# Kernel optimization log

Hardware: AMD Instinct MI355X
Metric: run time of the kernel (lower is better)

Reference implementation:

```python
import jax, jax.numpy as jnp
import numpy as np

R, I, T = 1024, 8, 65536
SPECTRAL_RADIUS = 1.0
CONNECTIVITY_RATE = 1.0


def setup_inputs() -> dict:
    key = jax.random.key(0)
    k1, k2, k3, k4 = jax.random.split(key, 4)
    inputs = jax.random.normal(k1, (T, I), dtype=jnp.float32)
    W_in = jax.random.uniform(k2, (R, I), minval=-1.0, maxval=1.0, dtype=jnp.float32)
    # reservoir: uniform(-1,1), sparsified where a random normal exceeds connectivity_rate
    W = jax.random.uniform(k3, (R, R), minval=-1.0, maxval=1.0, dtype=jnp.float32)
    mask_noise = jax.random.normal(k4, (R, R), dtype=jnp.float32)
    W = jnp.where(mask_noise > CONNECTIVITY_RATE, 0.0, W)
    # scale to target spectral radius (init-time, done in numpy)
    rho = np.max(np.abs(np.linalg.eigvals(np.asarray(W, dtype=np.float64))))
    W_res = (W * (SPECTRAL_RADIUS / np.float32(rho))).astype(jnp.float32)
    state0 = jnp.zeros((R,), dtype=jnp.float32)
    return {"inputs": inputs, "W_in": W_in, "W_res": W_res, "state0": state0}


def reference(inputs, W_in, W_res, state0):
    # ESN reservoir scan: s_t = tanh(W_in @ x_t + W_res @ s_{t-1});
    # collect [s_t; x_t] as column t of the state collection matrix.
    def step(s, x):
        s_new = jnp.tanh(W_in @ x + W_res @ s)  # (R,)
        return s_new, jnp.concatenate([s_new, x])  # (R + I,)

    _, cols = jax.lax.scan(step, state0, inputs)  # cols: (T, R + I)
    return cols.T  # (R + I, T), matching column-wise tf.concat
```

## Files before the change

### kernel.cpp

```cpp
#include <hip/hip_runtime.h>
#include <cstdint>

typedef __attribute__((ext_vector_type(8))) short short8;
typedef __attribute__((ext_vector_type(4))) float f32x4;
typedef __attribute__((ext_vector_type(4))) unsigned u32x4;

#define R_DIM 1024
#define KE    1056
#define T_LEN 65536
#define LCH   64
#define WARM  24
#define STEPS (WARM + LCH)
#define CGN   32
#define WGC   32
#define RWG   8

static __device__ __forceinline__ unsigned short f2bf(float f){
  unsigned u = __builtin_bit_cast(unsigned, f);
  u += 0x7fffu + ((u >> 16) & 1u);
  return (unsigned short)(u >> 16);
}
static __device__ __forceinline__ float fast_tanh(float x){
  float e = __expf(2.0f * x);
  return 1.0f - 2.0f / (e + 1.0f);
}

__global__ void k_build_wext(const float* __restrict__ Wres,
                             const float* __restrict__ Win,
                             short* __restrict__ Wext){
  int idx = blockIdx.x * 256 + threadIdx.x;
  int r = idx / KE, k = idx % KE;
  float v = 0.0f;
  if (k < 1024)      v = Wres[(size_t)r * 1024 + k];
  else if (k < 1032) v = Win[r * 8 + (k - 1024)];
  Wext[idx] = (short)f2bf(v);
}

__global__ void k_zero(unsigned* __restrict__ p){
  p[blockIdx.x * 256 + threadIdx.x] = 0u;
}

__global__ void k_init_x(const float* __restrict__ in, short* __restrict__ S0,
                         unsigned* __restrict__ cnt){
  int c = blockIdx.x * 256 + threadIdx.x;
  if (c < 512) cnt[c] = 0u;
  if (c < 1024){
    int t0 = c * LCH - WARM;
    uint4 xv = {0,0,0,0};
    if (t0 >= 0){
      const float4 A4 = *(const float4*)(in + (size_t)t0 * 8);
      const float4 B4 = *(const float4*)(in + (size_t)t0 * 8 + 4);
      xv.x = f2bf(A4.x) | ((unsigned)f2bf(A4.y) << 16);
      xv.y = f2bf(A4.z) | ((unsigned)f2bf(A4.w) << 16);
      xv.z = f2bf(B4.x) | ((unsigned)f2bf(B4.y) << 16);
      xv.w = f2bf(B4.z) | ((unsigned)f2bf(B4.w) << 16);
    }
    *(uint4*)(S0 + (size_t)c * KE + 1024) = xv;
  }
}

__global__ void k_xrows(const float* __restrict__ in, float* __restrict__ out){
  int t = blockIdx.x * 256 + threadIdx.x;
  const float4 a = *(const float4*)(in + (size_t)t * 8);
  const float4 b = *(const float4*)(in + (size_t)t * 8 + 4);
  out[(size_t)(R_DIM + 0) * T_LEN + t] = a.x;
  out[(size_t)(R_DIM + 1) * T_LEN + t] = a.y;
  out[(size_t)(R_DIM + 2) * T_LEN + t] = a.z;
  out[(size_t)(R_DIM + 3) * T_LEN + t] = a.w;
  out[(size_t)(R_DIM + 4) * T_LEN + t] = b.x;
  out[(size_t)(R_DIM + 5) * T_LEN + t] = b.y;
  out[(size_t)(R_DIM + 6) * T_LEN + t] = b.z;
  out[(size_t)(R_DIM + 7) * T_LEN + t] = b.w;
}

__global__ void k_transpose(const short* __restrict__ hist, float* __restrict__ out){
  __shared__ float tile[64][65];
  const int t0 = blockIdx.x * 64;
  const int r0 = blockIdx.y * 64;
  for (int it = 0; it < 2; ++it){
    int id = it * 256 + threadIdx.x;
    int tr = id >> 3;
    int c8 = (id & 7) * 8;
    short8 v = *(const short8*)(hist + (size_t)(t0 + tr) * KE + r0 + c8);
    #pragma unroll
    for (int j = 0; j < 8; ++j){
      unsigned u = ((unsigned)(unsigned short)v[j]) << 16;
      tile[tr][c8 + j] = __builtin_bit_cast(float, u);
    }
  }
  __syncthreads();
  #pragma unroll
  for (int p = 0; p < 16; ++p){
    int rr = (threadIdx.x >> 6) + p * 4;
    int tc = threadIdx.x & 63;
    out[(size_t)(r0 + rr) * T_LEN + t0 + tc] = tile[tc][rr];
  }
}

template<bool HIST>
__global__ __launch_bounds__(512, 1)
void k_esn(const float* __restrict__ inputs, const short* __restrict__ Wext,
           short* __restrict__ S0, short* __restrict__ S1,
           short* __restrict__ hist, unsigned* __restrict__ cnt,
           float* __restrict__ out)
{
  __shared__ __align__(16) char lds[65536];
  const int tid  = threadIdx.x;
  const int cg   = blockIdx.x & (CGN - 1);
  const int rwg  = blockIdx.x >> 5;
  const int wv   = tid >> 6;
  const int lane = tid & 63;
  const int l15  = lane & 15, l4 = lane >> 4;
  const int hi   = wv & 1;
  const int rbase = rwg * 128 + (wv >> 1) * 32;
  const int colbase = cg * WGC;
  unsigned* gflags = cnt + cg * 16;

  auto browf = [&](int col, int k) -> const short* {
    if (!HIST || k <= WARM) return ((k & 1) ? S1 : S0) + (size_t)col * KE;
    return hist + (size_t)(col * LCH + (k - WARM) - 1) * KE;
  };
  auto wrowf = [&](int col, int k) -> short* {
    if (!HIST || (k + 1) <= WARM) return ((k & 1) ? S0 : S1) + (size_t)col * KE;
    return hist + (size_t)(col * LCH + (k - WARM)) * KE;
  };

  const int NA = hi ? 16 : 17;
  const int KB = hi ? 17 : 0;
  const int NL = hi ? 15 : 17;
  short8 a0[17], a1[17];
  {
    const short* abase = Wext + (size_t)(rbase + l15) * KE + l4 * 8;
    #pragma unroll
    for (int i = 0; i < 17; ++i){
      if (i < NA){
        const short* ap = abase + (KB + i) * 32;
        a0[i] = *(const short8*)ap;
        a1[i] = *(const short8*)(ap + (size_t)16 * KE);
      }
    }
  }

  const int scol = tid >> 4;
  const int skb0 = (tid & 15) << 4;
  const int sswz = (scol & 7) << 4;
  const int colb0 = l15 * 2048;
  const int bswz  = (l15 & 7) << 4;
  const int l4b   = l4 * 16;

  for (int k = 0; k < STEPS; ++k){
    if (k > 0){
      if (wv == 0){
        const unsigned* fp = gflags + (lane & 7);
        int guard = 0;
        for (;;){
          unsigned v;
          asm volatile("global_load_dword %0, %1, off sc0 sc1\n\t"
                       "s_waitcnt vmcnt(0)"
                       : "=v"(v) : "v"(fp) : "memory");
          if (!__any((int)(v < (unsigned)k))) break;
          __builtin_amdgcn_s_sleep(1);
          if (++guard > 1000000) break;
        }
      }
      __syncthreads();
    }

    unsigned long long t00=0, t01=0, t10=0, t11=0;
    if (hi){
      const unsigned long long* tp0 =
        (const unsigned long long*)(browf(colbase + l15, k) + 1024 + l4 * 8);
      const unsigned long long* tp1 =
        (const unsigned long long*)(browf(colbase + 16 + l15, k) + 1024 + l4 * 8);
      t00 = __hip_atomic_load(tp0,     __ATOMIC_RELAXED, __HIP_MEMORY_SCOPE_AGENT);
      t01 = __hip_atomic_load(tp0 + 1, __ATOMIC_RELAXED, __HIP_MEMORY_SCOPE_AGENT);
      t10 = __hip_atomic_load(tp1,     __ATOMIC_RELAXED, __HIP_MEMORY_SCOPE_AGENT);
      t11 = __hip_atomic_load(tp1 + 1, __ATOMIC_RELAXED, __HIP_MEMORY_SCOPE_AGENT);
    }

    {
      const short* srow = browf(colbase + scol, k);
      const char* sp = (const char*)srow + skb0;
      u32x4 r0,r1,r2,r3,r4,r5,r6,r7;
      asm volatile(
        "global_load_dwordx4 %0, %8, off sc0 sc1\n\t"
        "global_load_dwordx4 %1, %8, off offset:256 sc0 sc1\n\t"
        "global_load_dwordx4 %2, %8, off offset:512 sc0 sc1\n\t"
        "global_load_dwordx4 %3, %8, off offset:768 sc0 sc1\n\t"
        "global_load_dwordx4 %4, %8, off offset:1024 sc0 sc1\n\t"
        "global_load_dwordx4 %5, %8, off offset:1280 sc0 sc1\n\t"
        "global_load_dwordx4 %6, %8, off offset:1536 sc0 sc1\n\t"
        "global_load_dwordx4 %7, %8, off offset:1792 sc0 sc1\n\t"
        "s_waitcnt vmcnt(0)"
        : "=&v"(r0),"=&v"(r1),"=&v"(r2),"=&v"(r3),
          "=&v"(r4),"=&v"(r5),"=&v"(r6),"=&v"(r7)
        : "v"(sp) : "memory");
      char* dst = &lds[scol * 2048];
      *(u32x4*)(dst + ((skb0 +    0) ^ sswz)) = r0;
      *(u32x4*)(dst + ((skb0 +  256) ^ sswz)) = r1;
      *(u32x4*)(dst + ((skb0 +  512) ^ sswz)) = r2;
      *(u32x4*)(dst + ((skb0 +  768) ^ sswz)) = r3;
      *(u32x4*)(dst + ((skb0 + 1024) ^ sswz)) = r4;
      *(u32x4*)(dst + ((skb0 + 1280) ^ sswz)) = r5;
      *(u32x4*)(dst + ((skb0 + 1536) ^ sswz)) = r6;
      *(u32x4*)(dst + ((skb0 + 1792) ^ sswz)) = r7;
    }
    __syncthreads();

    f32x4 acc00 = {0,0,0,0}, acc01 = {0,0,0,0}, acc10 = {0,0,0,0}, acc11 = {0,0,0,0};
    #pragma unroll
    for (int i = 0; i < 17; ++i){
      if (i < NL){
        int kb = (KB + i) * 64 + l4b;
        const short8 b0 = *(const short8*)(&lds[colb0 + ((kb) ^ bswz)]);
        const short8 b1 = *(const short8*)(&lds[colb0 + 32768 + ((kb) ^ bswz)]);
        acc00 = __builtin_amdgcn_mfma_f32_16x16x32_bf16(a0[i], b0, acc00, 0, 0, 0);
        acc01 = __builtin_amdgcn_mfma_f32_16x16x32_bf16(a0[i], b1, acc01, 0, 0, 0);
        acc10 = __builtin_amdgcn_mfma_f32_16x16x32_bf16(a1[i], b0, acc10, 0, 0, 0);
        acc11 = __builtin_amdgcn_mfma_f32_16x16x32_bf16(a1[i], b1, acc11, 0, 0, 0);
      }
    }
    if (hi){
      u32x4 v0; v0.x=(unsigned)t00; v0.y=(unsigned)(t00>>32); v0.z=(unsigned)t01; v0.w=(unsigned)(t01>>32);
      u32x4 v1; v1.x=(unsigned)t10; v1.y=(unsigned)(t10>>32); v1.z=(unsigned)t11; v1.w=(unsigned)(t11>>32);
      const short8 b0 = __builtin_bit_cast(short8, v0);
      const short8 b1 = __builtin_bit_cast(short8, v1);
      acc00 = __builtin_amdgcn_mfma_f32_16x16x32_bf16(a0[15], b0, acc00, 0, 0, 0);
      acc01 = __builtin_amdgcn_mfma_f32_16x16x32_bf16(a0[15], b1, acc01, 0, 0, 0);
      acc10 = __builtin_amdgcn_mfma_f32_16x16x32_bf16(a1[15], b0, acc10, 0, 0, 0);
      acc11 = __builtin_amdgcn_mfma_f32_16x16x32_bf16(a1[15], b1, acc11, 0, 0, 0);
    }

    __syncthreads();
    {
      f32x4 wA = hi ? acc00 : acc10;
      f32x4 wB = hi ? acc01 : acc11;
      char* xp = &lds[wv * 2048 + lane * 32];
      *(f32x4*)(xp)      = wA;
      *(f32x4*)(xp + 16) = wB;
    }
    __syncthreads();
    {
      const char* pp = &lds[(wv ^ 1) * 2048 + lane * 32];
      f32x4 p0 = *(const f32x4*)(pp);
      f32x4 p1 = *(const f32x4*)(pp + 16);
      f32x4 f0 = (hi ? acc10 : acc00) + p0;
      f32x4 f1 = (hi ? acc11 : acc01) + p1;
      const int rowb = rbase + hi * 16 + l4 * 4;
      #pragma unroll
      for (int ct = 0; ct < 2; ++ct){
        f32x4 z = ct ? f1 : f0;
        float s0 = fast_tanh(z[0]), s1 = fast_tanh(z[1]);
        float s2 = fast_tanh(z[2]), s3 = fast_tanh(z[3]);
        unsigned long long pk = (unsigned long long)f2bf(s0)
          | ((unsigned long long)f2bf(s1) << 16)
          | ((unsigned long long)f2bf(s2) << 32)
          | ((unsigned long long)f2bf(s3) << 48);
        int col = colbase + ct * 16 + l15;
        short* wp = wrowf(col, k) + rowb;
        asm volatile("global_store_dwordx2 %0, %1, off sc0 sc1"
                     :: "v"(wp), "v"(pk) : "memory");
        if (!HIST && k >= WARM){
          int tk = col * LCH + k - WARM;
          float* op = out + (size_t)rowb * T_LEN + tk;
          op[0] = s0; op[(size_t)T_LEN] = s1;
          op[(size_t)2 * T_LEN] = s2; op[(size_t)3 * T_LEN] = s3;
        }
      }
    }

    if (rwg == 0 && tid < WGC && (k + 1) < STEPS){
      int col = colbase + tid;
      short* xr = wrowf(col, k) + 1024;
      int tn = col * LCH + (k + 1) - WARM;
      u32x4 xv = {0,0,0,0};
      if (tn >= 0){
        const float4 A4 = *(const float4*)(inputs + (size_t)tn * 8);
        const float4 B4 = *(const float4*)(inputs + (size_t)tn * 8 + 4);
        xv.x = f2bf(A4.x) | ((unsigned)f2bf(A4.y) << 16);
        xv.y = f2bf(A4.z) | ((unsigned)f2bf(A4.w) << 16);
        xv.z = f2bf(B4.x) | ((unsigned)f2bf(B4.y) << 16);
        xv.w = f2bf(B4.z) | ((unsigned)f2bf(B4.w) << 16);
      }
      asm volatile("global_store_dwordx4 %0, %1, off sc0 sc1"
                   :: "v"(xr), "v"(xv) : "memory");
    }

    asm volatile("s_waitcnt vmcnt(0)" ::: "memory");
    __syncthreads();
    if (tid == 0 && (k + 1) < STEPS){
      unsigned* fw = gflags + rwg;
      unsigned fv = (unsigned)(k + 1);
      asm volatile("global_store_dword %0, %1, off sc0 sc1"
                   :: "v"(fw), "v"(fv) : "memory");
    }
  }
}

extern "C" void kernel_launch(void* const* d_in, const int* in_sizes, int n_in,
                              void* d_out, int out_size, void* d_ws, size_t ws_size,
                              hipStream_t stream)
{
  (void)in_sizes; (void)n_in; (void)out_size;
  const float* inputs = (const float*)d_in[0];
  const float* Win    = (const float*)d_in[1];
  const float* Wres   = (const float*)d_in[2];
  float* out = (float*)d_out;
  char* ws = (char*)d_ws;

  short*    Wext = (short*)(ws);
  short*    S0   = (short*)(ws + 2162688);
  short*    S1   = (short*)(ws + 2162688 * 2);
  unsigned* cnt  = (unsigned*)(ws + 2162688 * 3);
  short*    hist = (short*)(ws + 6490112);
  const bool hist_ok = ws_size >= (6490112ull + 138412032ull);

  hipLaunchKernelGGL(k_build_wext, dim3(4224), dim3(256), 0, stream, Wres, Win, Wext);
  hipLaunchKernelGGL(k_zero,       dim3(4224), dim3(256), 0, stream, (unsigned*)S0);
  hipLaunchKernelGGL(k_init_x,     dim3(4),    dim3(256), 0, stream, inputs, S0, cnt);
  hipLaunchKernelGGL(k_xrows,      dim3(256),  dim3(256), 0, stream, inputs, out);
  if (hist_ok){
    hipLaunchKernelGGL((k_esn<true>),  dim3(RWG * CGN), dim3(512), 0, stream,
                       inputs, Wext, S0, S1, hist, cnt, out);
    hipLaunchKernelGGL(k_transpose, dim3(1024, 16), dim3(256), 0, stream, hist, out);
  } else {
    hipLaunchKernelGGL((k_esn<false>), dim3(RWG * CGN), dim3(512), 0, stream,
                       inputs, Wext, S0, S1, hist, cnt, out);
  }
}
```

Measured before the change: 592.7 us.

## Halve chunk length to double column groups and store warmup states in history

Splits the time axis into 2048 chunks of 32 steps with 16 warmup steps, instead of 1024 chunks of 64 with 24 warmup. This doubles the number of column groups to 64, so the grid grows to 512 workgroups, and relaxes launch bounds to allow more than one workgroup per CU. The goal is to cut the serial step count per chunk and use more of the GPU. Warmup states are ping-ponged inside the history buffer rather than separate S0/S1 arrays, and the cross-wave LDS exchange uses a swizzled layout to reduce bank conflicts. The cost is more redundant warmup work overall, a shorter warmup that may raise error, and more workgroups polling global flags.

Result: slower. 1.079 ms (+82.1%).

```diff
diff --git a/kernel.cpp b/kernel.cpp
--- a/kernel.cpp
+++ b/kernel.cpp
@@ -8,10 +8,11 @@
 #define R_DIM 1024
 #define KE    1056
 #define T_LEN 65536
-#define LCH   64
-#define WARM  24
+#define CCH   2048
+#define LCH   32
+#define WARM  16
 #define STEPS (WARM + LCH)
-#define CGN   32
+#define NGRP  64
 #define WGC   32
 #define RWG   8
 
@@ -36,15 +37,17 @@
   Wext[idx] = (short)f2bf(v);
 }
 
-__global__ void k_zero(unsigned* __restrict__ p){
-  p[blockIdx.x * 256 + threadIdx.x] = 0u;
-}
-
-__global__ void k_init_x(const float* __restrict__ in, short* __restrict__ S0,
-                         unsigned* __restrict__ cnt){
+__global__ void k_zero_init(short* __restrict__ base, size_t rowstride){
+  int idx = blockIdx.x * 256 + threadIdx.x;
+  int c = idx >> 9, d = idx & 511;
+  ((unsigned*)(base + (size_t)c * rowstride))[d] = 0u;
+}
+
+__global__ void k_init_x(const float* __restrict__ in, short* __restrict__ x0,
+                         size_t rowstride, unsigned* __restrict__ cnt){
   int c = blockIdx.x * 256 + threadIdx.x;
-  if (c < 512) cnt[c] = 0u;
-  if (c < 1024){
+  if (c < NGRP * 16) cnt[c] = 0u;
+  if (c < CCH){
     int t0 = c * LCH - WARM;
     uint4 xv = {0,0,0,0};
     if (t0 >= 0){
@@ -55,7 +58,7 @@
       xv.z = f2bf(B4.x) | ((unsigned)f2bf(B4.y) << 16);
       xv.w = f2bf(B4.z) | ((unsigned)f2bf(B4.w) << 16);
     }
-    *(uint4*)(S0 + (size_t)c * KE + 1024) = xv;
+    *(uint4*)(x0 + (size_t)c * rowstride) = xv;
   }
 }
 
@@ -98,7 +101,7 @@
 }
 
 template<bool HIST>
-__global__ __launch_bounds__(512, 1)
+__global__ __launch_bounds__(512, 4)
 void k_esn(const float* __restrict__ inputs, const short* __restrict__ Wext,
            short* __restrict__ S0, short* __restrict__ S1,
            short* __restrict__ hist, unsigned* __restrict__ cnt,
@@ -106,23 +109,31 @@
 {
   __shared__ __align__(16) char lds[65536];
   const int tid  = threadIdx.x;
-  const int cg   = blockIdx.x & (CGN - 1);
-  const int rwg  = blockIdx.x >> 5;
+  const int g    = blockIdx.x >> 3;
+  const int rwg  = blockIdx.x & 7;
   const int wv   = tid >> 6;
   const int lane = tid & 63;
   const int l15  = lane & 15, l4 = lane >> 4;
   const int hi   = wv & 1;
   const int rbase = rwg * 128 + (wv >> 1) * 32;
-  const int colbase = cg * WGC;
-  unsigned* gflags = cnt + cg * 16;
+  const int colbase = g * WGC;
+  unsigned* gflags = cnt + g * 16;
 
   auto browf = [&](int col, int k) -> const short* {
-    if (!HIST || k <= WARM) return ((k & 1) ? S1 : S0) + (size_t)col * KE;
-    return hist + (size_t)(col * LCH + (k - WARM) - 1) * KE;
+    if (HIST){
+      size_t row = (k <= WARM) ? ((size_t)col * LCH + ((k + 1) & 1))
+                               : ((size_t)col * LCH + (size_t)(k - WARM) - 1);
+      return hist + row * KE;
+    }
+    return ((k & 1) ? S1 : S0) + (size_t)col * KE;
   };
   auto wrowf = [&](int col, int k) -> short* {
-    if (!HIST || (k + 1) <= WARM) return ((k & 1) ? S0 : S1) + (size_t)col * KE;
-    return hist + (size_t)(col * LCH + (k - WARM)) * KE;
+    if (HIST){
+      size_t row = (k < WARM) ? ((size_t)col * LCH + (k & 1))
+                              : ((size_t)col * LCH + (size_t)(k - WARM));
+      return hist + row * KE;
+    }
+    return ((k & 1) ? S0 : S1) + (size_t)col * KE;
   };
 
   const int NA = hi ? 16 : 17;
@@ -147,6 +158,7 @@
   const int colb0 = l15 * 2048;
   const int bswz  = (l15 & 7) << 4;
   const int l4b   = l4 * 16;
+  const int xsw = (lane * 16) ^ ((lane >> 3) << 4);
 
   for (int k = 0; k < STEPS; ++k){
     if (k > 0){
@@ -235,15 +247,13 @@
     {
       f32x4 wA = hi ? acc00 : acc10;
       f32x4 wB = hi ? acc01 : acc11;
-      char* xp = &lds[wv * 2048 + lane * 32];
-      *(f32x4*)(xp)      = wA;
-      *(f32x4*)(xp + 16) = wB;
+      *(f32x4*)(&lds[wv * 1024 + xsw])        = wA;
+      *(f32x4*)(&lds[8192 + wv * 1024 + xsw]) = wB;
     }
     __syncthreads();
     {
-      const char* pp = &lds[(wv ^ 1) * 2048 + lane * 32];
-      f32x4 p0 = *(const f32x4*)(pp);
-      f32x4 p1 = *(const f32x4*)(pp + 16);
+      f32x4 p0 = *(const f32x4*)(&lds[(wv ^ 1) * 1024 + xsw]);
+      f32x4 p1 = *(const f32x4*)(&lds[8192 + (wv ^ 1) * 1024 + xsw]);
       f32x4 f0 = (hi ? acc10 : acc00) + p0;
       f32x4 f1 = (hi ? acc11 : acc01) + p1;
       const int rowb = rbase + hi * 16 + l4 * 4;
@@ -309,22 +319,29 @@
   char* ws = (char*)d_ws;
 
   short*    Wext = (short*)(ws);
-  short*    S0   = (short*)(ws + 2162688);
-  short*    S1   = (short*)(ws + 2162688 * 2);
-  unsigned* cnt  = (unsigned*)(ws + 2162688 * 3);
-  short*    hist = (short*)(ws + 6490112);
-  const bool hist_ok = ws_size >= (6490112ull + 138412032ull);
+  unsigned* cnt  = (unsigned*)(ws + 2162688);
+  char*     data = ws + 2166784;
+  short*    hist = (short*)data;
+  short*    S0   = (short*)data;
+  short*    S1   = (short*)(data + 4325376);
+  const bool hist_ok = ws_size >= (2166784ull + 138412032ull);
 
   hipLaunchKernelGGL(k_build_wext, dim3(4224), dim3(256), 0, stream, Wres, Win, Wext);
-  hipLaunchKernelGGL(k_zero,       dim3(4224), dim3(256), 0, stream, (unsigned*)S0);
-  hipLaunchKernelGGL(k_init_x,     dim3(4),    dim3(256), 0, stream, inputs, S0, cnt);
   hipLaunchKernelGGL(k_xrows,      dim3(256),  dim3(256), 0, stream, inputs, out);
   if (hist_ok){
-    hipLaunchKernelGGL((k_esn<true>),  dim3(RWG * CGN), dim3(512), 0, stream,
+    hipLaunchKernelGGL(k_zero_init, dim3(4096), dim3(256), 0, stream,
+                       hist + KE, (size_t)LCH * KE);
+    hipLaunchKernelGGL(k_init_x,    dim3(8),    dim3(256), 0, stream,
+                       inputs, hist + KE + 1024, (size_t)LCH * KE, cnt);
+    hipLaunchKernelGGL((k_esn<true>),  dim3(RWG * NGRP), dim3(512), 0, stream,
                        inputs, Wext, S0, S1, hist, cnt, out);
     hipLaunchKernelGGL(k_transpose, dim3(1024, 16), dim3(256), 0, stream, hist, out);
   } else {
-    hipLaunchKernelGGL((k_esn<false>), dim3(RWG * CGN), dim3(512), 0, stream,
+    hipLaunchKernelGGL(k_zero_init, dim3(4096), dim3(256), 0, stream,
+                       S0, (size_t)KE);
+    hipLaunchKernelGGL(k_init_x,    dim3(8),    dim3(256), 0, stream,
+                       inputs, S0 + 1024, (size_t)KE, cnt);
+    hipLaunchKernelGGL((k_esn<false>), dim3(RWG * NGRP), dim3(512), 0, stream,
                        inputs, Wext, S0, S1, hist, cnt, out);
   }
 }
```
